# Optimization experiments

Hardware: AMD Instinct MI355X
Metric: run time of the kernel (lower is better)

The kernel has to match this reference:

```python
import jax, jax.numpy as jnp
import numpy as np
from jax import lax

B, T, PRED_LEN = 1024, 100, 30
E, H, IN = 512, 1024, 2


def _gru_cell(h, gx, Whh, bhh):
    # PyTorch GRU cell. gx = x @ Wih.T + bih precomputed, shape (B, 3H).
    gh = h @ Whh.T + bhh
    gx_r, gx_z, gx_n = jnp.split(gx, 3, axis=-1)
    gh_r, gh_z, gh_n = jnp.split(gh, 3, axis=-1)
    r = jax.nn.sigmoid(gx_r + gh_r)
    z = jax.nn.sigmoid(gx_z + gh_z)
    n = jnp.tanh(gx_n + r * gh_n)
    return (1.0 - z) * n + z * h


def _run_gru(x, h0, Wih, Whh, bih, bhh):
    # x: (B, T, F) -> outputs (B, T, H), final hidden (B, H)
    gx = jnp.einsum('btf,gf->btg', x, Wih) + bih  # batch all input projections
    def step(h, gxt):
        h_new = _gru_cell(h, gxt, Whh, bhh)
        return h_new, h_new
    h_last, ys = lax.scan(step, h0, jnp.swapaxes(gx, 0, 1))
    return jnp.swapaxes(ys, 0, 1), h_last


def setup_inputs() -> dict:
    key = jax.random.key(0)
    ks = iter(jax.random.split(key, 32))
    s = 1.0 / np.sqrt(H)
    u = lambda k, shp: jax.random.uniform(k, shp, jnp.float32, -s, s)
    inp = {'obs': jax.random.normal(next(ks), (B, T, IN), jnp.float32)}
    inp['We'] = u(next(ks), (E, IN)); inp['be'] = u(next(ks), (E,))
    inp['Wed'] = u(next(ks), (E, 2)); inp['bed'] = u(next(ks), (E,))
    for name, fin in [('enc1', E), ('enc2', H), ('dec1', E), ('dec2', H)]:
        inp[name + '_Wih'] = u(next(ks), (3 * H, fin))
        inp[name + '_Whh'] = u(next(ks), (3 * H, H))
        inp[name + '_bih'] = u(next(ks), (3 * H,))
        inp[name + '_bhh'] = u(next(ks), (3 * H,))
    inp['Wout'] = u(next(ks), (2, H)); inp['bout'] = u(next(ks), (2,))
    return inp


def reference(obs, We, be, Wed, bed,
              enc1_Wih, enc1_Whh, enc1_bih, enc1_bhh,
              enc2_Wih, enc2_Whh, enc2_bih, enc2_bhh,
              dec1_Wih, dec1_Whh, dec1_bih, dec1_bhh,
              dec2_Wih, dec2_Whh, dec2_bih, dec2_bhh,
              Wout, bout):
    b = obs.shape[0]
    h0 = jnp.zeros((b, H), obs.dtype)
    # --- encoder ---
    emb = jnp.tanh(jnp.einsum('bti,ei->bte', obs, We) + be)
    enc1, h = _run_gru(emb, h0, enc1_Wih, enc1_Whh, enc1_bih, enc1_bhh)
    # quirk preserved: hidden from gru1 is fed as h0 of gru2
    enc2, h = _run_gru(enc1, h, enc2_Wih, enc2_Whh, enc2_bih, enc2_bhh)
    out_loc0 = enc2[:, -2, :] @ Wout.T + bout  # second-to-last step (B, 2)
    def dec_step(carry, _):
        hc, last = carry
        d_emb = jnp.tanh(last @ Wed.T + bed)
        h1 = _gru_cell(hc, d_emb @ dec1_Wih.T + dec1_bih, dec1_Whh, dec1_bhh)
        h2 = _gru_cell(h1, h1 @ dec2_Wih.T + dec2_bih, dec2_Whh, dec2_bhh)
        out = h2 @ Wout.T + bout
        return (h2, out), out
    _, preds = lax.scan(dec_step, (h, out_loc0), None, length=PRED_LEN)
    return jnp.swapaxes(preds, 0, 1)  # (B, pred_len, 2)
```

## Files before the change

### kernel.cpp

```cpp
#include <hip/hip_runtime.h>
#include <stdint.h>

#define NB 1024
#define NT 100
#define NPRED 30
#define NE 512
#define NH 1024
#define NG (3*NH)

typedef unsigned short u16;
typedef unsigned int u32;
typedef u16 u16x4 __attribute__((ext_vector_type(4)));
typedef float f32x4 __attribute__((ext_vector_type(4)));
typedef __bf16 bf16x8 __attribute__((ext_vector_type(8)));

__device__ __forceinline__ u16 f2b(float f){
  u32 u = __float_as_uint(f);
  u = (u + 0x7FFFu + ((u >> 16) & 1u)) >> 16;
  return (u16)u;
}
__device__ __forceinline__ float sig_(float x){ return 1.0f/(1.0f+__expf(-x)); }
__device__ __forceinline__ float tanh_(float x){
  float e = __expf(2.0f*fabsf(x));
  return copysignf(1.0f - 2.0f/(e+1.0f), x);
}

__global__ void cvt_kernel(const float* src, u16* dst, int n4){
  int i = blockIdx.x*256 + threadIdx.x;
  if (i < n4){
    f32x4 v = ((const f32x4*)src)[i];
    u16x4 o;
    o[0]=f2b(v[0]); o[1]=f2b(v[1]); o[2]=f2b(v[2]); o[3]=f2b(v[3]);
    ((u16x4*)dst)[i] = o;
  }
}

__global__ void emb_kernel(const float* __restrict__ obs, const float* __restrict__ We,
                           const float* __restrict__ be, u16* __restrict__ out, int t){
  int idx = blockIdx.x*256 + threadIdx.x;
  int b = idx >> 9, e = idx & 511;
  float x0 = obs[(b*NT + t)*2], x1 = obs[(b*NT + t)*2 + 1];
  out[idx] = f2b(tanh_(We[e*2]*x0 + We[e*2+1]*x1 + be[e]));
}

__global__ void demb_kernel(const float* __restrict__ last, const float* __restrict__ Wed,
                            const float* __restrict__ bed, u16* __restrict__ out){
  int idx = blockIdx.x*256 + threadIdx.x;
  int b = idx >> 9, e = idx & 511;
  out[idx] = f2b(tanh_(Wed[e*2]*last[b*2] + Wed[e*2+1]*last[b*2+1] + bed[e]));
}

__device__ __forceinline__ void gload16(const u16* g, const u16* lds){
  __builtin_amdgcn_global_load_lds(
      (const __attribute__((address_space(1))) void*)g,
      (__attribute__((address_space(3))) void*)lds, 16, 0, 0);
}

__device__ __forceinline__ void gemm_tile_body(
    const u16* __restrict__ A, int lda,
    const u16* __restrict__ W, int K,
    const float* __restrict__ bias, float* __restrict__ C,
    int bRow, int bCol)
{
  __shared__ __align__(16) u16 As[2][128][64];
  __shared__ __align__(16) u16 Bs[2][128][64];

  const int tid = threadIdx.x;
  const int w = tid >> 6, l = tid & 63;
  const int wm = w >> 1, wn = w & 1;
  const int fr = l & 15, lhi = l >> 4;
  const int srow = l >> 3;
  const int gcol = (((l & 7) ^ srow) * 8);

  f32x4 acc[4][4];
  #pragma unroll
  for (int m=0;m<4;m++)
    #pragma unroll
    for (int n=0;n<4;n++) acc[m][n] = (f32x4)0.0f;

  const u16* Ab = A + (size_t)bRow*lda + gcol;
  const u16* Wb = W + (size_t)bCol*K + gcol;
  const int NK = K >> 6;

  #pragma unroll
  for (int s4=0;s4<4;s4++){
    int slab = w*4 + s4;
    int row = slab*8 + srow;
    gload16(Ab + (size_t)row*lda, &As[0][slab*8][0]);
    gload16(Wb + (size_t)row*K,   &Bs[0][slab*8][0]);
  }
  __syncthreads();

  for (int t = 0; t < NK; ++t){
    const int cur = t & 1;
    if (t + 1 < NK){
      const int k0 = (t+1)*64;
      #pragma unroll
      for (int s4=0;s4<4;s4++){
        int slab = w*4 + s4;
        int row = slab*8 + srow;
        gload16(Ab + (size_t)row*lda + k0, &As[cur^1][slab*8][0]);
        gload16(Wb + (size_t)row*K   + k0, &Bs[cur^1][slab*8][0]);
      }
    }
    const u16* Ac = &As[cur][0][0];
    const u16* Bc = &Bs[cur][0][0];
    #pragma unroll
    for (int kk=0; kk<2; ++kk){
      const int ch = (((kk*4 + lhi) ^ (l & 7)) * 8);
      bf16x8 af[4], bfr[4];
      #pragma unroll
      for (int m=0;m<4;m++)
        af[m] = *(const bf16x8*)(Ac + (size_t)(wm*64 + m*16 + fr)*64 + ch);
      #pragma unroll
      for (int n=0;n<4;n++)
        bfr[n] = *(const bf16x8*)(Bc + (size_t)(wn*64 + n*16 + fr)*64 + ch);
      #pragma unroll
      for (int m=0;m<4;m++)
        #pragma unroll
        for (int n=0;n<4;n++)
          acc[m][n] = __builtin_amdgcn_mfma_f32_16x16x32_bf16(af[m], bfr[n], acc[m][n], 0, 0, 0);
    }
    __syncthreads();
  }

  const int crow = lhi * 4, ccol = l & 15;
  #pragma unroll
  for (int n=0;n<4;n++){
    int col = bCol + wn*64 + n*16 + ccol;
    float bv = bias[col];
    #pragma unroll
    for (int m=0;m<4;m++){
      int row = bRow + wm*64 + m*16 + crow;
      float* Cp = C + (size_t)row*NG + col;
      #pragma unroll
      for (int r=0;r<4;r++) Cp[(size_t)r*NG] = acc[m][n][r] + bv;
    }
  }
}

__global__ __launch_bounds__(256)
void gemm_dual_kernel(
  const u16* A0, int lda0, int K0, const u16* W0, const float* bias0, float* C0,
  const u16* A1, int lda1, int K1, const u16* W1, const float* bias1, float* C1)
{
  if (blockIdx.z == 0)
    gemm_tile_body(A0, lda0, W0, K0, bias0, C0, blockIdx.y*128, blockIdx.x*128);
  else
    gemm_tile_body(A1, lda1, W1, K1, bias1, C1, blockIdx.y*128, blockIdx.x*128);
}

__global__ void gru_cell_kernel(const float* __restrict__ gx, const float* __restrict__ gh,
                                const float* __restrict__ hin, float* __restrict__ hout,
                                u16* __restrict__ houtb, u16* __restrict__ seq)
{
  int idx = blockIdx.x*256 + threadIdx.x;
  int b = idx >> 8, jq = idx & 255;
  int base = b*768;
  const f32x4* gx4 = (const f32x4*)gx;
  const f32x4* gh4 = (const f32x4*)gh;
  f32x4 xr = gx4[base + jq], xz = gx4[base + 256 + jq], xn = gx4[base + 512 + jq];
  f32x4 hr = gh4[base + jq], hz = gh4[base + 256 + jq], hn = gh4[base + 512 + jq];
  f32x4 hv = ((const f32x4*)hin)[idx];
  f32x4 o; u16x4 ob;
  #pragma unroll
  for (int c=0;c<4;c++){
    float r = sig_(xr[c] + hr[c]);
    float z = sig_(xz[c] + hz[c]);
    float n = tanh_(xn[c] + r*hn[c]);
    float h = (1.0f - z)*n + z*hv[c];
    o[c] = h; ob[c] = f2b(h);
  }
  ((f32x4*)hout)[idx] = o;
  ((u16x4*)houtb)[idx] = ob;
  if (seq) ((u16x4*)seq)[idx] = ob;
}

__global__ void outproj_kernel(const float* __restrict__ h, const float* __restrict__ Wout,
                               const float* __restrict__ bout, float* __restrict__ last,
                               float* __restrict__ dout, int t)
{
  int b = blockIdx.x, tid = threadIdx.x;
  float s0 = 0.f, s1 = 0.f;
  const float* hb_ = h + (size_t)b*NH;
  for (int j = tid; j < NH; j += 256){
    float hv = hb_[j];
    s0 += hv * Wout[j];
    s1 += hv * Wout[NH + j];
  }
  #pragma unroll
  for (int off = 32; off > 0; off >>= 1){
    s0 += __shfl_down(s0, off);
    s1 += __shfl_down(s1, off);
  }
  __shared__ float red[8];
  int w = tid >> 6;
  if ((tid & 63) == 0){ red[w*2] = s0; red[w*2+1] = s1; }
  __syncthreads();
  if (tid == 0){
    float o0 = red[0]+red[2]+red[4]+red[6] + bout[0];
    float o1 = red[1]+red[3]+red[5]+red[7] + bout[1];
    last[b*2]   = o0;
    last[b*2+1] = o1;
    if (dout){ dout[(size_t)b*(NPRED*2) + t*2]     = o0;
               dout[(size_t)b*(NPRED*2) + t*2 + 1] = o1; }
  }
}

extern "C" void kernel_launch(void* const* d_in, const int* in_sizes, int n_in,
                              void* d_out, int out_size, void* d_ws, size_t ws_size,
                              hipStream_t stream)
{
  (void)in_sizes; (void)n_in; (void)out_size;
  const float* obs  = (const float*)d_in[0];
  const float* We   = (const float*)d_in[1];
  const float* be   = (const float*)d_in[2];
  const float* Wed  = (const float*)d_in[3];
  const float* bed  = (const float*)d_in[4];
  const float* e1Wih = (const float*)d_in[5];
  const float* e1Whh = (const float*)d_in[6];
  const float* e1bih = (const float*)d_in[7];
  const float* e1bhh = (const float*)d_in[8];
  const float* e2Wih = (const float*)d_in[9];
  const float* e2Whh = (const float*)d_in[10];
  const float* e2bih = (const float*)d_in[11];
  const float* e2bhh = (const float*)d_in[12];
  const float* d1Wih = (const float*)d_in[13];
  const float* d1Whh = (const float*)d_in[14];
  const float* d1bih = (const float*)d_in[15];
  const float* d1bhh = (const float*)d_in[16];
  const float* d2Wih = (const float*)d_in[17];
  const float* d2Whh = (const float*)d_in[18];
  const float* d2bih = (const float*)d_in[19];
  const float* d2bhh = (const float*)d_in[20];
  const float* Wout = (const float*)d_in[21];
  const float* bout = (const float*)d_in[22];
  float* out = (float*)d_out;

  char* ws = (char*)d_ws;
  size_t off = 0;
  auto alloc = [&](size_t bytes)->char* {
    char* p = ws + off;
    off += (bytes + 255) & ~(size_t)255;
    return p;
  };
  u16* wE1i = (u16*)alloc((size_t)NG*NE*2);
  u16* wE1h = (u16*)alloc((size_t)NG*NH*2);
  u16* wE2i = (u16*)alloc((size_t)NG*NH*2);
  u16* wE2h = (u16*)alloc((size_t)NG*NH*2);
  u16* wD1i = (u16*)alloc((size_t)NG*NE*2);
  u16* wD1h = (u16*)alloc((size_t)NG*NH*2);
  u16* wD2i = (u16*)alloc((size_t)NG*NH*2);
  u16* wD2h = (u16*)alloc((size_t)NG*NH*2);
  u16* embb  = (u16*)alloc((size_t)NB*NE*2);
  float* h1f = (float*)alloc((size_t)NB*NH*4);
  u16*   h1b = (u16*)alloc((size_t)NB*NH*2);
  float* h2f = (float*)alloc((size_t)NB*NH*4);
  u16*   h2b = (u16*)alloc((size_t)NB*NH*2);
  float* gx  = (float*)alloc((size_t)NB*NG*4);
  float* gh  = (float*)alloc((size_t)NB*NG*4);
  float* last = (float*)alloc((size_t)NB*2*4);

  const size_t slot = (size_t)NB*NH*2;
  size_t avail = (ws_size > off + (1u<<20)) ? (ws_size - off - (1u<<20)) : 0;
  int cs = (int)(avail / slot);
  if (cs > NT) cs = NT;
  u16* cache = (u16*)alloc((size_t)cs * slot);
  const int cache_start = NT - cs;

  hipMemsetAsync(h1f, 0, (size_t)NB*NH*4, stream);
  hipMemsetAsync(h1b, 0, (size_t)NB*NH*2, stream);

  auto cvt = [&](const float* src, u16* dst, size_t n){
    int n4 = (int)(n >> 2);
    cvt_kernel<<<dim3((n4 + 255)/256), dim3(256), 0, stream>>>(src, dst, n4);
  };
  cvt(e1Wih, wE1i, (size_t)NG*NE);
  cvt(e1Whh, wE1h, (size_t)NG*NH);
  cvt(e2Wih, wE2i, (size_t)NG*NH);
  cvt(e2Whh, wE2h, (size_t)NG*NH);
  cvt(d1Wih, wD1i, (size_t)NG*NE);
  cvt(d1Whh, wD1h, (size_t)NG*NH);
  cvt(d2Wih, wD2i, (size_t)NG*NH);
  cvt(d2Whh, wD2h, (size_t)NG*NH);

  const dim3 blk(256);
  const dim3 dual_grid(NG/128, NB/128, 2);
  const dim3 emb_grid((NB*NE)/256);
  const dim3 cell_grid((NB*NH/4)/256);

  for (int t = 0; t < NT; ++t){
    emb_kernel<<<emb_grid, blk, 0, stream>>>(obs, We, be, embb, t);
    gemm_dual_kernel<<<dual_grid, blk, 0, stream>>>(
        embb, NE, NE, wE1i, e1bih, gx,
        h1b,  NH, NH, wE1h, e1bhh, gh);
    u16* slot_p = (t >= cache_start) ? cache + (size_t)(t - cache_start)*NB*NH : (u16*)nullptr;
    gru_cell_kernel<<<cell_grid, blk, 0, stream>>>(gx, gh, h1f, h1f, h1b, slot_p);
  }

  hipMemcpyAsync(h2f, h1f, (size_t)NB*NH*4, hipMemcpyDeviceToDevice, stream);
  hipMemcpyAsync(h2b, h1b, (size_t)NB*NH*2, hipMemcpyDeviceToDevice, stream);

  if (cache_start > 0){
    hipMemsetAsync(h1f, 0, (size_t)NB*NH*4, stream);
    hipMemsetAsync(h1b, 0, (size_t)NB*NH*2, stream);
  }
  for (int t = 0; t < cache_start; ++t){
    emb_kernel<<<emb_grid, blk, 0, stream>>>(obs, We, be, embb, t);
    gemm_dual_kernel<<<dual_grid, blk, 0, stream>>>(
        embb, NE, NE, wE1i, e1bih, gx,
        h1b,  NH, NH, wE1h, e1bhh, gh);
    gru_cell_kernel<<<cell_grid, blk, 0, stream>>>(gx, gh, h1f, h1f, h1b, (u16*)nullptr);
    gemm_dual_kernel<<<dual_grid, blk, 0, stream>>>(
        h1b, NH, NH, wE2i, e2bih, gx,
        h2b, NH, NH, wE2h, e2bhh, gh);
    gru_cell_kernel<<<cell_grid, blk, 0, stream>>>(gx, gh, h2f, h2f, h2b, (u16*)nullptr);
    if (t == NT - 2)
      outproj_kernel<<<dim3(NB), blk, 0, stream>>>(h2f, Wout, bout, last, (float*)nullptr, 0);
  }
  for (int t = cache_start; t < NT; ++t){
    const u16* enc1_t = cache + (size_t)(t - cache_start)*NB*NH;
    gemm_dual_kernel<<<dual_grid, blk, 0, stream>>>(
        enc1_t, NH, NH, wE2i, e2bih, gx,
        h2b,    NH, NH, wE2h, e2bhh, gh);
    gru_cell_kernel<<<cell_grid, blk, 0, stream>>>(gx, gh, h2f, h2f, h2b, (u16*)nullptr);
    if (t == NT - 2)
      outproj_kernel<<<dim3(NB), blk, 0, stream>>>(h2f, Wout, bout, last, (float*)nullptr, 0);
  }

  for (int t = 0; t < NPRED; ++t){
    demb_kernel<<<emb_grid, blk, 0, stream>>>(last, Wed, bed, embb);
    gemm_dual_kernel<<<dual_grid, blk, 0, stream>>>(
        embb, NE, NE, wD1i, d1bih, gx,
        h2b,  NH, NH, wD1h, d1bhh, gh);
    gru_cell_kernel<<<cell_grid, blk, 0, stream>>>(gx, gh, h2f, h1f, h1b, (u16*)nullptr);
    gemm_dual_kernel<<<dual_grid, blk, 0, stream>>>(
        h1b, NH, NH, wD2i, d2bih, gx,
        h1b, NH, NH, wD2h, d2bhh, gh);
    gru_cell_kernel<<<cell_grid, blk, 0, stream>>>(gx, gh, h1f, h2f, h2b, (u16*)nullptr);
    outproj_kernel<<<dim3(NB), blk, 0, stream>>>(h2f, Wout, bout, last, out, t);
  }
}
```

Before: 8.357 ms.

## Use 4-stage K=32 LDS pipeline with vmcnt waits in GEMM tile

Replaces the double-buffered K=64 tile loop with a four-buffer K=32 pipeline that keeps three global-to-LDS loads in flight. Each step uses an explicit s_waitcnt vmcnt plus one barrier instead of two __syncthreads. A new XOR swizzle is applied for the 32-wide rows. The aim is to hide global load latency better in the input-projection GEMMs, at the cost of more barriers per K and fragile hand-counted vmcnt values.

```diff
diff --git a/kernel.cpp b/kernel.cpp
--- a/kernel.cpp
+++ b/kernel.cpp
@@ -62,15 +62,22 @@
     const float* __restrict__ bias, float* __restrict__ C,
     int bRow, int bCol)
 {
-  __shared__ __align__(16) u16 As[2][128][64];
-  __shared__ __align__(16) u16 Bs[2][128][64];
+  __shared__ __align__(16) u16 As[4][128][32];
+  __shared__ __align__(16) u16 Bs[4][128][32];
 
   const int tid = threadIdx.x;
   const int w = tid >> 6, l = tid & 63;
   const int wm = w >> 1, wn = w & 1;
   const int fr = l & 15, lhi = l >> 4;
-  const int srow = l >> 3;
-  const int gcol = (((l & 7) ^ srow) * 8);
+
+  const int srow = l >> 2;
+  const int sch  = (((l & 3) ^ ((l >> 2) & 3) ^ (l >> 4)) << 3);
+  const int s0 = w*2, s1 = w*2 + 1;
+
+  const u16* A0p = A + (size_t)(bRow + s0*16 + srow)*lda + sch;
+  const u16* A1p = A + (size_t)(bRow + s1*16 + srow)*lda + sch;
+  const u16* W0p = W + (size_t)(bCol + s0*16 + srow)*K + sch;
+  const u16* W1p = W + (size_t)(bCol + s1*16 + srow)*K + sch;
 
   f32x4 acc[4][4];
   #pragma unroll
@@ -78,51 +85,55 @@
     #pragma unroll
     for (int n=0;n<4;n++) acc[m][n] = (f32x4)0.0f;
 
-  const u16* Ab = A + (size_t)bRow*lda + gcol;
-  const u16* Wb = W + (size_t)bCol*K + gcol;
-  const int NK = K >> 6;
-
-  #pragma unroll
-  for (int s4=0;s4<4;s4++){
-    int slab = w*4 + s4;
-    int row = slab*8 + srow;
-    gload16(Ab + (size_t)row*lda, &As[0][slab*8][0]);
-    gload16(Wb + (size_t)row*K,   &Bs[0][slab*8][0]);
-  }
-  __syncthreads();
-
-  for (int t = 0; t < NK; ++t){
-    const int cur = t & 1;
-    if (t + 1 < NK){
-      const int k0 = (t+1)*64;
-      #pragma unroll
-      for (int s4=0;s4<4;s4++){
-        int slab = w*4 + s4;
-        int row = slab*8 + srow;
-        gload16(Ab + (size_t)row*lda + k0, &As[cur^1][slab*8][0]);
-        gload16(Wb + (size_t)row*K   + k0, &Bs[cur^1][slab*8][0]);
-      }
-    }
-    const u16* Ac = &As[cur][0][0];
-    const u16* Bc = &Bs[cur][0][0];
-    #pragma unroll
-    for (int kk=0; kk<2; ++kk){
-      const int ch = (((kk*4 + lhi) ^ (l & 7)) * 8);
-      bf16x8 af[4], bfr[4];
-      #pragma unroll
-      for (int m=0;m<4;m++)
-        af[m] = *(const bf16x8*)(Ac + (size_t)(wm*64 + m*16 + fr)*64 + ch);
-      #pragma unroll
-      for (int n=0;n<4;n++)
-        bfr[n] = *(const bf16x8*)(Bc + (size_t)(wn*64 + n*16 + fr)*64 + ch);
-      #pragma unroll
-      for (int m=0;m<4;m++)
-        #pragma unroll
-        for (int n=0;n<4;n++)
-          acc[m][n] = __builtin_amdgcn_mfma_f32_16x16x32_bf16(af[m], bfr[n], acc[m][n], 0, 0, 0);
-    }
-    __syncthreads();
-  }
+  const int rch = ((lhi ^ (fr & 3) ^ (fr >> 2)) << 3);
+
+  #define STAGE(buf, t) do { int _k = (t) << 5; \
+    gload16(A0p + _k, &As[(buf)][s0*16][0]); \
+    gload16(A1p + _k, &As[(buf)][s1*16][0]); \
+    gload16(W0p + _k, &Bs[(buf)][s0*16][0]); \
+    gload16(W1p + _k, &Bs[(buf)][s1*16][0]); } while(0)
+
+  #define COMPUTE(buf) do { \
+    const u16* Ac = &As[(buf)][0][0]; \
+    const u16* Bc = &Bs[(buf)][0][0]; \
+    bf16x8 af[4], bfr[4]; \
+    _Pragma("unroll") \
+    for (int m=0;m<4;m++) af[m]  = *(const bf16x8*)(Ac + (size_t)(wm*64 + m*16 + fr)*32 + rch); \
+    _Pragma("unroll") \
+    for (int n=0;n<4;n++) bfr[n] = *(const bf16x8*)(Bc + (size_t)(wn*64 + n*16 + fr)*32 + rch); \
+    _Pragma("unroll") \
+    for (int m=0;m<4;m++) \
+      _Pragma("unroll") \
+      for (int n=0;n<4;n++) \
+        acc[m][n] = __builtin_amdgcn_mfma_f32_16x16x32_bf16(af[m], bfr[n], acc[m][n], 0, 0, 0); \
+    } while(0)
+
+  const int NK = K >> 5;
+
+  STAGE(0, 0); STAGE(1, 1); STAGE(2, 2);
+
+  for (int t = 0; t + 4 <= NK; ++t){
+    asm volatile("s_waitcnt vmcnt(8)" ::: "memory");
+    __builtin_amdgcn_s_barrier();
+    asm volatile("" ::: "memory");
+    STAGE((t + 3) & 3, t + 3);
+    COMPUTE(t & 3);
+  }
+  asm volatile("s_waitcnt vmcnt(8)" ::: "memory");
+  __builtin_amdgcn_s_barrier();
+  asm volatile("" ::: "memory");
+  COMPUTE((NK - 3) & 3);
+  asm volatile("s_waitcnt vmcnt(4)" ::: "memory");
+  __builtin_amdgcn_s_barrier();
+  asm volatile("" ::: "memory");
+  COMPUTE((NK - 2) & 3);
+  asm volatile("s_waitcnt vmcnt(0)" ::: "memory");
+  __builtin_amdgcn_s_barrier();
+  asm volatile("" ::: "memory");
+  COMPUTE((NK - 1) & 3);
+
+  #undef STAGE
+  #undef COMPUTE
 
   const int crow = lhi * 4, ccol = l & 15;
   #pragma unroll
```

Result: slower. 10.02 ms (+19.9%).

## Fuse GRU gate GEMMs and cell update into one kernel with gate-interleaved weights

Applied to the files above, without the earlier changes.

Weights are repacked so that each 384-column block holds the r, z and n gate rows for the same 128 hidden units. This lets one kernel run both the input and hidden GEMMs into register accumulators and apply the GRU cell in its epilogue. The fp32 gx/gh intermediates and the separate cell kernel go away, and the embedding and decoder-embedding computations are folded into the step and output-projection kernels. Hidden-state buffers are double-buffered to avoid read/write races across blocks. The grid drops to only 128 blocks, each holding 32 accumulators, which may leave much of the GPU idle.

```diff
diff --git a/kernel.cpp b/kernel.cpp
--- a/kernel.cpp
+++ b/kernel.cpp
@@ -25,14 +25,27 @@
   return copysignf(1.0f - 2.0f/(e+1.0f), x);
 }
 
-__global__ void cvt_kernel(const float* src, u16* dst, int n4){
-  int i = blockIdx.x*256 + threadIdx.x;
-  if (i < n4){
-    f32x4 v = ((const f32x4*)src)[i];
-    u16x4 o;
-    o[0]=f2b(v[0]); o[1]=f2b(v[1]); o[2]=f2b(v[2]); o[3]=f2b(v[3]);
-    ((u16x4*)dst)[i] = o;
-  }
+__global__ void pack_w_kernel(const float* __restrict__ src, u16* __restrict__ dst, int K){
+  int idx = blockIdx.x*256 + threadIdx.x;
+  int kq = K >> 2;
+  int rowp = idx / kq, kc = idx % kq;
+  int q = rowp / 48, rem = rowp % 48;
+  int g = rem >> 4, s = rem & 15;
+  int j = q*16 + s;
+  f32x4 v = ((const f32x4*)src)[(size_t)(g*NH + j)*kq + kc];
+  u16x4 o;
+  o[0]=f2b(v[0]); o[1]=f2b(v[1]); o[2]=f2b(v[2]); o[3]=f2b(v[3]);
+  ((u16x4*)dst)[idx] = o;
+}
+
+__global__ void pack_bias_kernel(const float* __restrict__ bih, const float* __restrict__ bhh,
+                                 float* __restrict__ PB1, float* __restrict__ PB2){
+  int idx = blockIdx.x*256 + threadIdx.x;
+  int q = idx / 48, rem = idx % 48;
+  int g = rem >> 4, s = rem & 15;
+  int j = q*16 + s;
+  PB1[idx] = (g < 2) ? (bih[g*NH + j] + bhh[g*NH + j]) : bhh[2*NH + j];
+  if (idx < NH) PB2[idx] = bih[2*NH + idx];
 }
 
 __global__ void emb_kernel(const float* __restrict__ obs, const float* __restrict__ We,
@@ -43,150 +56,147 @@
   out[idx] = f2b(tanh_(We[e*2]*x0 + We[e*2+1]*x1 + be[e]));
 }
 
-__global__ void demb_kernel(const float* __restrict__ last, const float* __restrict__ Wed,
-                            const float* __restrict__ bed, u16* __restrict__ out){
-  int idx = blockIdx.x*256 + threadIdx.x;
-  int b = idx >> 9, e = idx & 511;
-  out[idx] = f2b(tanh_(Wed[e*2]*last[b*2] + Wed[e*2+1]*last[b*2+1] + bed[e]));
-}
-
 __device__ __forceinline__ void gload16(const u16* g, const u16* lds){
   __builtin_amdgcn_global_load_lds(
       (const __attribute__((address_space(1))) void*)g,
       (__attribute__((address_space(3))) void*)lds, 16, 0, 0);
 }
 
-__device__ __forceinline__ void gemm_tile_body(
-    const u16* __restrict__ A, int lda,
-    const u16* __restrict__ W, int K,
-    const float* __restrict__ bias, float* __restrict__ C,
-    int bRow, int bCol)
+template<bool TOX>
+__device__ __forceinline__ void gemm_phase(
+    const u16* __restrict__ A, int lda, int K,
+    const u16* __restrict__ W,
+    int rb, int w, int l,
+    f32x4* acc, f32x4* accx,
+    u16 (*As)[64][64], u16 (*Ws)[384][64])
 {
-  __shared__ __align__(16) u16 As[2][128][64];
-  __shared__ __align__(16) u16 Bs[2][128][64];
-
-  const int tid = threadIdx.x;
-  const int w = tid >> 6, l = tid & 63;
-  const int wm = w >> 1, wn = w & 1;
   const int fr = l & 15, lhi = l >> 4;
   const int srow = l >> 3;
   const int gcol = (((l & 7) ^ srow) * 8);
-
-  f32x4 acc[4][4];
-  #pragma unroll
-  for (int m=0;m<4;m++)
-    #pragma unroll
-    for (int n=0;n<4;n++) acc[m][n] = (f32x4)0.0f;
-
-  const u16* Ab = A + (size_t)bRow*lda + gcol;
-  const u16* Wb = W + (size_t)bCol*K + gcol;
+  const u16* Ab = A + (size_t)(rb*64)*lda + gcol;
+  const u16* Wb = W + gcol;
   const int NK = K >> 6;
 
-  #pragma unroll
-  for (int s4=0;s4<4;s4++){
-    int slab = w*4 + s4;
-    int row = slab*8 + srow;
-    gload16(Ab + (size_t)row*lda, &As[0][slab*8][0]);
-    gload16(Wb + (size_t)row*K,   &Bs[0][slab*8][0]);
-  }
+  #define STAGE_P(buf, kt) do { int _k0 = (kt)*64; \
+    _Pragma("unroll") \
+    for (int c=0;c<2;c++){ int sl = w*2 + c; \
+      gload16(Ab + (size_t)(sl*8+srow)*lda + _k0, &As[(buf)][sl*8][0]); } \
+    _Pragma("unroll") \
+    for (int c=0;c<12;c++){ int sl = w*12 + c; \
+      gload16(Wb + (size_t)(sl*8+srow)*K + _k0, &Ws[(buf)][sl*8][0]); } } while(0)
+
+  STAGE_P(0, 0);
   __syncthreads();
 
   for (int t = 0; t < NK; ++t){
     const int cur = t & 1;
-    if (t + 1 < NK){
-      const int k0 = (t+1)*64;
-      #pragma unroll
-      for (int s4=0;s4<4;s4++){
-        int slab = w*4 + s4;
-        int row = slab*8 + srow;
-        gload16(Ab + (size_t)row*lda + k0, &As[cur^1][slab*8][0]);
-        gload16(Wb + (size_t)row*K   + k0, &Bs[cur^1][slab*8][0]);
-      }
-    }
-    const u16* Ac = &As[cur][0][0];
-    const u16* Bc = &Bs[cur][0][0];
+    if (t + 1 < NK) STAGE_P(cur^1, t+1);
     #pragma unroll
     for (int kk=0; kk<2; ++kk){
       const int ch = (((kk*4 + lhi) ^ (l & 7)) * 8);
-      bf16x8 af[4], bfr[4];
+      bf16x8 af[4], wf[6];
       #pragma unroll
       for (int m=0;m<4;m++)
-        af[m] = *(const bf16x8*)(Ac + (size_t)(wm*64 + m*16 + fr)*64 + ch);
+        af[m] = *(const bf16x8*)(&As[cur][m*16 + fr][0] + ch);
       #pragma unroll
-      for (int n=0;n<4;n++)
-        bfr[n] = *(const bf16x8*)(Bc + (size_t)(wn*64 + n*16 + fr)*64 + ch);
+      for (int nf=0;nf<6;nf++)
+        wf[nf] = *(const bf16x8*)(&Ws[cur][w*96 + nf*16 + fr][0] + ch);
       #pragma unroll
-      for (int m=0;m<4;m++)
+      for (int nf=0;nf<6;nf++)
         #pragma unroll
-        for (int n=0;n<4;n++)
-          acc[m][n] = __builtin_amdgcn_mfma_f32_16x16x32_bf16(af[m], bfr[n], acc[m][n], 0, 0, 0);
+        for (int m=0;m<4;m++){
+          if (TOX && (nf % 3) == 2)
+            accx[(nf/3)*4 + m] = __builtin_amdgcn_mfma_f32_16x16x32_bf16(af[m], wf[nf], accx[(nf/3)*4 + m], 0, 0, 0);
+          else
+            acc[nf*4 + m] = __builtin_amdgcn_mfma_f32_16x16x32_bf16(af[m], wf[nf], acc[nf*4 + m], 0, 0, 0);
+        }
     }
     __syncthreads();
   }
-
-  const int crow = lhi * 4, ccol = l & 15;
-  #pragma unroll
-  for (int n=0;n<4;n++){
-    int col = bCol + wn*64 + n*16 + ccol;
-    float bv = bias[col];
+  #undef STAGE_P
+}
+
+__global__ __launch_bounds__(256)
+void fused_step(
+    const u16* __restrict__ Ax, int ldax, int Kx, const u16* __restrict__ Wx,
+    const u16* __restrict__ Ah, const u16* __restrict__ Wh,
+    const float* __restrict__ PB1, const float* __restrict__ PB2,
+    const float* __restrict__ hin, float* __restrict__ houtf,
+    u16* __restrict__ houtb, u16* __restrict__ seq,
+    const float* __restrict__ obs, const float* __restrict__ We,
+    const float* __restrict__ be, u16* __restrict__ embb, int et)
+{
+  __shared__ __align__(16) u16 As[2][64][64];
+  __shared__ __align__(16) u16 Ws[2][384][64];
+
+  const int rb = blockIdx.x >> 3, cb = blockIdx.x & 7;
+  const int tid = threadIdx.x, w = tid >> 6, l = tid & 63;
+  const int s = l & 15, lhi = l >> 4;
+
+  f32x4 acc[24], accx[8];
+  #pragma unroll
+  for (int i=0;i<24;i++) acc[i] = (f32x4)0.0f;
+  #pragma unroll
+  for (int i=0;i<8;i++) accx[i] = (f32x4)0.0f;
+
+  gemm_phase<true >(Ax, ldax, Kx, Wx + (size_t)(cb*384)*Kx, rb, w, l, acc, accx, As, Ws);
+  gemm_phase<false>(Ah, NH,   NH, Wh + (size_t)(cb*384)*NH, rb, w, l, acc, accx, As, Ws);
+
+  #pragma unroll
+  for (int gi=0; gi<2; ++gi){
+    int j = cb*128 + (2*w + gi)*16 + s;
+    int pbase = cb*384 + w*96 + gi*48 + s;
+    float pbr = PB1[pbase], pbz = PB1[pbase + 16], pbn = PB1[pbase + 32];
+    float pb2 = PB2[j];
     #pragma unroll
     for (int m=0;m<4;m++){
-      int row = bRow + wm*64 + m*16 + crow;
-      float* Cp = C + (size_t)row*NG + col;
       #pragma unroll
-      for (int r=0;r<4;r++) Cp[(size_t)r*NG] = acc[m][n][r] + bv;
+      for (int r=0;r<4;r++){
+        int row = rb*64 + m*16 + lhi*4 + r;
+        size_t hoff = (size_t)row*NH + j;
+        float rpre = acc[(gi*3+0)*4 + m][r] + pbr;
+        float zpre = acc[(gi*3+1)*4 + m][r] + pbz;
+        float nh   = acc[(gi*3+2)*4 + m][r] + pbn;
+        float nx   = accx[gi*4 + m][r] + pb2;
+        float r_ = sig_(rpre), z_ = sig_(zpre);
+        float nn = tanh_(nx + r_*nh);
+        float h = (1.0f - z_)*nn + z_*hin[hoff];
+        houtf[hoff] = h;
+        u16 hb = f2b(h);
+        houtb[hoff] = hb;
+        if (seq) seq[hoff] = hb;
+      }
     }
   }
-}
-
-__global__ __launch_bounds__(256)
-void gemm_dual_kernel(
-  const u16* A0, int lda0, int K0, const u16* W0, const float* bias0, float* C0,
-  const u16* A1, int lda1, int K1, const u16* W1, const float* bias1, float* C1)
-{
-  if (blockIdx.z == 0)
-    gemm_tile_body(A0, lda0, W0, K0, bias0, C0, blockIdx.y*128, blockIdx.x*128);
-  else
-    gemm_tile_body(A1, lda1, W1, K1, bias1, C1, blockIdx.y*128, blockIdx.x*128);
-}
-
-__global__ void gru_cell_kernel(const float* __restrict__ gx, const float* __restrict__ gh,
-                                const float* __restrict__ hin, float* __restrict__ hout,
-                                u16* __restrict__ houtb, u16* __restrict__ seq)
-{
-  int idx = blockIdx.x*256 + threadIdx.x;
-  int b = idx >> 8, jq = idx & 255;
-  int base = b*768;
-  const f32x4* gx4 = (const f32x4*)gx;
-  const f32x4* gh4 = (const f32x4*)gh;
-  f32x4 xr = gx4[base + jq], xz = gx4[base + 256 + jq], xn = gx4[base + 512 + jq];
-  f32x4 hr = gh4[base + jq], hz = gh4[base + 256 + jq], hn = gh4[base + 512 + jq];
-  f32x4 hv = ((const f32x4*)hin)[idx];
-  f32x4 o; u16x4 ob;
-  #pragma unroll
-  for (int c=0;c<4;c++){
-    float r = sig_(xr[c] + hr[c]);
-    float z = sig_(xz[c] + hz[c]);
-    float n = tanh_(xn[c] + r*hn[c]);
-    float h = (1.0f - z)*n + z*hv[c];
-    o[c] = h; ob[c] = f2b(h);
-  }
-  ((f32x4*)hout)[idx] = o;
-  ((u16x4*)houtb)[idx] = ob;
-  if (seq) ((u16x4*)seq)[idx] = ob;
-}
-
-__global__ void outproj_kernel(const float* __restrict__ h, const float* __restrict__ Wout,
-                               const float* __restrict__ bout, float* __restrict__ last,
-                               float* __restrict__ dout, int t)
+
+  if (embb){
+    int row = rb*64 + (tid >> 2);
+    float x0 = obs[((size_t)row*NT + et)*2];
+    float x1 = obs[((size_t)row*NT + et)*2 + 1];
+    #pragma unroll
+    for (int c=0;c<8;c++){
+      int e = cb*64 + ((tid & 3)*8 + c)*2;
+      u16 v0 = f2b(tanh_(We[e*2]  *x0 + We[e*2+1]*x1 + be[e]));
+      u16 v1 = f2b(tanh_(We[e*2+2]*x0 + We[e*2+3]*x1 + be[e+1]));
+      ((u32*)embb)[(size_t)row*256 + cb*32 + (tid & 3)*8 + c] = (u32)v0 | ((u32)v1 << 16);
+    }
+  }
+}
+
+__global__ void outproj_demb_kernel(const float* __restrict__ h,
+                                    const float* __restrict__ Wout, const float* __restrict__ bout,
+                                    float* __restrict__ dout, int ot,
+                                    const float* __restrict__ Wed, const float* __restrict__ bed,
+                                    u16* __restrict__ dembb)
 {
   int b = blockIdx.x, tid = threadIdx.x;
+  f32x4 hv = ((const f32x4*)h)[b*256 + tid];
+  int j0 = tid*4;
   float s0 = 0.f, s1 = 0.f;
-  const float* hb_ = h + (size_t)b*NH;
-  for (int j = tid; j < NH; j += 256){
-    float hv = hb_[j];
-    s0 += hv * Wout[j];
-    s1 += hv * Wout[NH + j];
+  #pragma unroll
+  for (int c=0;c<4;c++){
+    s0 += hv[c]*Wout[j0+c];
+    s1 += hv[c]*Wout[NH + j0 + c];
   }
   #pragma unroll
   for (int off = 32; off > 0; off >>= 1){
@@ -194,17 +204,23 @@
     s1 += __shfl_down(s1, off);
   }
   __shared__ float red[8];
+  __shared__ float lastsh[2];
   int w = tid >> 6;
   if ((tid & 63) == 0){ red[w*2] = s0; red[w*2+1] = s1; }
   __syncthreads();
   if (tid == 0){
     float o0 = red[0]+red[2]+red[4]+red[6] + bout[0];
     float o1 = red[1]+red[3]+red[5]+red[7] + bout[1];
-    last[b*2]   = o0;
-    last[b*2+1] = o1;
-    if (dout){ dout[(size_t)b*(NPRED*2) + t*2]     = o0;
-               dout[(size_t)b*(NPRED*2) + t*2 + 1] = o1; }
-  }
+    lastsh[0] = o0; lastsh[1] = o1;
+    if (dout){ dout[(size_t)b*(NPRED*2) + ot*2]     = o0;
+               dout[(size_t)b*(NPRED*2) + ot*2 + 1] = o1; }
+  }
+  __syncthreads();
+  float x0 = lastsh[0], x1 = lastsh[1];
+  int e0 = tid*2;
+  u16 v0 = f2b(tanh_(Wed[e0*2]  *x0 + Wed[e0*2+1]*x1 + bed[e0]));
+  u16 v1 = f2b(tanh_(Wed[e0*2+2]*x0 + Wed[e0*2+3]*x1 + bed[e0+1]));
+  ((u32*)dembb)[b*256 + tid] = (u32)v0 | ((u32)v1 << 16);
 }
 
 extern "C" void kernel_launch(void* const* d_in, const int* in_sizes, int n_in,
@@ -244,22 +260,24 @@
     off += (bytes + 255) & ~(size_t)255;
     return p;
   };
-  u16* wE1i = (u16*)alloc((size_t)NG*NE*2);
-  u16* wE1h = (u16*)alloc((size_t)NG*NH*2);
-  u16* wE2i = (u16*)alloc((size_t)NG*NH*2);
-  u16* wE2h = (u16*)alloc((size_t)NG*NH*2);
-  u16* wD1i = (u16*)alloc((size_t)NG*NE*2);
-  u16* wD1h = (u16*)alloc((size_t)NG*NH*2);
-  u16* wD2i = (u16*)alloc((size_t)NG*NH*2);
-  u16* wD2h = (u16*)alloc((size_t)NG*NH*2);
-  u16* embb  = (u16*)alloc((size_t)NB*NE*2);
+  u16* pE1i = (u16*)alloc((size_t)NG*NE*2);
+  u16* pE1h = (u16*)alloc((size_t)NG*NH*2);
+  u16* pE2i = (u16*)alloc((size_t)NG*NH*2);
+  u16* pE2h = (u16*)alloc((size_t)NG*NH*2);
+  u16* pD1i = (u16*)alloc((size_t)NG*NE*2);
+  u16* pD1h = (u16*)alloc((size_t)NG*NH*2);
+  u16* pD2i = (u16*)alloc((size_t)NG*NH*2);
+  u16* pD2h = (u16*)alloc((size_t)NG*NH*2);
+  float* PB1e1 = (float*)alloc(NG*4); float* PB2e1 = (float*)alloc(NH*4);
+  float* PB1e2 = (float*)alloc(NG*4); float* PB2e2 = (float*)alloc(NH*4);
+  float* PB1d1 = (float*)alloc(NG*4); float* PB2d1 = (float*)alloc(NH*4);
+  float* PB1d2 = (float*)alloc(NG*4); float* PB2d2 = (float*)alloc(NH*4);
+  u16* embbP[2] = { (u16*)alloc((size_t)NB*NE*2), (u16*)alloc((size_t)NB*NE*2) };
+  u16* dembb = (u16*)alloc((size_t)NB*NE*2);
   float* h1f = (float*)alloc((size_t)NB*NH*4);
-  u16*   h1b = (u16*)alloc((size_t)NB*NH*2);
+  u16*   h1bP[2] = { (u16*)alloc((size_t)NB*NH*2), (u16*)alloc((size_t)NB*NH*2) };
   float* h2f = (float*)alloc((size_t)NB*NH*4);
-  u16*   h2b = (u16*)alloc((size_t)NB*NH*2);
-  float* gx  = (float*)alloc((size_t)NB*NG*4);
-  float* gh  = (float*)alloc((size_t)NB*NG*4);
-  float* last = (float*)alloc((size_t)NB*2*4);
+  u16*   h2bP[2] = { (u16*)alloc((size_t)NB*NH*2), (u16*)alloc((size_t)NB*NH*2) };
 
   const size_t slot = (size_t)NB*NH*2;
   size_t avail = (ws_size > off + (1u<<20)) ? (ws_size - off - (1u<<20)) : 0;
@@ -269,75 +287,86 @@
   const int cache_start = NT - cs;
 
   hipMemsetAsync(h1f, 0, (size_t)NB*NH*4, stream);
-  hipMemsetAsync(h1b, 0, (size_t)NB*NH*2, stream);
-
-  auto cvt = [&](const float* src, u16* dst, size_t n){
-    int n4 = (int)(n >> 2);
-    cvt_kernel<<<dim3((n4 + 255)/256), dim3(256), 0, stream>>>(src, dst, n4);
+  hipMemsetAsync(h1bP[0], 0, (size_t)NB*NH*2, stream);
+
+  const dim3 blk(256);
+  auto packw = [&](const float* src, u16* dst, int K){
+    pack_w_kernel<<<dim3((NG*K/4)/256), blk, 0, stream>>>(src, dst, K);
   };
-  cvt(e1Wih, wE1i, (size_t)NG*NE);
-  cvt(e1Whh, wE1h, (size_t)NG*NH);
-  cvt(e2Wih, wE2i, (size_t)NG*NH);
-  cvt(e2Whh, wE2h, (size_t)NG*NH);
-  cvt(d1Wih, wD1i, (size_t)NG*NE);
-  cvt(d1Whh, wD1h, (size_t)NG*NH);
-  cvt(d2Wih, wD2i, (size_t)NG*NH);
-  cvt(d2Whh, wD2h, (size_t)NG*NH);
-
-  const dim3 blk(256);
-  const dim3 dual_grid(NG/128, NB/128, 2);
+  packw(e1Wih, pE1i, NE); packw(e1Whh, pE1h, NH);
+  packw(e2Wih, pE2i, NH); packw(e2Whh, pE2h, NH);
+  packw(d1Wih, pD1i, NE); packw(d1Whh, pD1h, NH);
+  packw(d2Wih, pD2i, NH); packw(d2Whh, pD2h, NH);
+  pack_bias_kernel<<<dim3(NG/256), blk, 0, stream>>>(e1bih, e1bhh, PB1e1, PB2e1);
+  pack_bias_kernel<<<dim3(NG/256), blk, 0, stream>>>(e2bih, e2bhh, PB1e2, PB2e2);
+  pack_bias_kernel<<<dim3(NG/256), blk, 0, stream>>>(d1bih, d1bhh, PB1d1, PB2d1);
+  pack_bias_kernel<<<dim3(NG/256), blk, 0, stream>>>(d2bih, d2bhh, PB1d2, PB2d2);
+
+  const dim3 fgrid(128);
   const dim3 emb_grid((NB*NE)/256);
-  const dim3 cell_grid((NB*NH/4)/256);
-
+
+  int p1 = 0, p2 = 0, pe = 0;
+
+  emb_kernel<<<emb_grid, blk, 0, stream>>>(obs, We, be, embbP[0], 0);
   for (int t = 0; t < NT; ++t){
-    emb_kernel<<<emb_grid, blk, 0, stream>>>(obs, We, be, embb, t);
-    gemm_dual_kernel<<<dual_grid, blk, 0, stream>>>(
-        embb, NE, NE, wE1i, e1bih, gx,
-        h1b,  NH, NH, wE1h, e1bhh, gh);
     u16* slot_p = (t >= cache_start) ? cache + (size_t)(t - cache_start)*NB*NH : (u16*)nullptr;
-    gru_cell_kernel<<<cell_grid, blk, 0, stream>>>(gx, gh, h1f, h1f, h1b, slot_p);
+    u16* embn = (t + 1 < NT) ? embbP[pe^1] : (u16*)nullptr;
+    fused_step<<<fgrid, blk, 0, stream>>>(
+        embbP[pe], NE, NE, pE1i, h1bP[p1], pE1h, PB1e1, PB2e1,
+        h1f, h1f, h1bP[p1^1], slot_p,
+        obs, We, be, embn, t+1);
+    p1 ^= 1; pe ^= 1;
   }
 
   hipMemcpyAsync(h2f, h1f, (size_t)NB*NH*4, hipMemcpyDeviceToDevice, stream);
-  hipMemcpyAsync(h2b, h1b, (size_t)NB*NH*2, hipMemcpyDeviceToDevice, stream);
+  hipMemcpyAsync(h2bP[0], h1bP[p1], (size_t)NB*NH*2, hipMemcpyDeviceToDevice, stream);
+  p2 = 0;
 
   if (cache_start > 0){
     hipMemsetAsync(h1f, 0, (size_t)NB*NH*4, stream);
-    hipMemsetAsync(h1b, 0, (size_t)NB*NH*2, stream);
+    hipMemsetAsync(h1bP[0], 0, (size_t)NB*NH*2, stream);
+    p1 = 0; pe = 0;
+    emb_kernel<<<emb_grid, blk, 0, stream>>>(obs, We, be, embbP[0], 0);
   }
   for (int t = 0; t < cache_start; ++t){
-    emb_kernel<<<emb_grid, blk, 0, stream>>>(obs, We, be, embb, t);
-    gemm_dual_kernel<<<dual_grid, blk, 0, stream>>>(
-        embb, NE, NE, wE1i, e1bih, gx,
-        h1b,  NH, NH, wE1h, e1bhh, gh);
-    gru_cell_kernel<<<cell_grid, blk, 0, stream>>>(gx, gh, h1f, h1f, h1b, (u16*)nullptr);
-    gemm_dual_kernel<<<dual_grid, blk, 0, stream>>>(
-        h1b, NH, NH, wE2i, e2bih, gx,
-        h2b, NH, NH, wE2h, e2bhh, gh);
-    gru_cell_kernel<<<cell_grid, blk, 0, stream>>>(gx, gh, h2f, h2f, h2b, (u16*)nullptr);
+    u16* embn = (t + 1 < cache_start) ? embbP[pe^1] : (u16*)nullptr;
+    fused_step<<<fgrid, blk, 0, stream>>>(
+        embbP[pe], NE, NE, pE1i, h1bP[p1], pE1h, PB1e1, PB2e1,
+        h1f, h1f, h1bP[p1^1], (u16*)nullptr,
+        obs, We, be, embn, t+1);
+    p1 ^= 1; pe ^= 1;
+    fused_step<<<fgrid, blk, 0, stream>>>(
+        h1bP[p1], NH, NH, pE2i, h2bP[p2], pE2h, PB1e2, PB2e2,
+        h2f, h2f, h2bP[p2^1], (u16*)nullptr,
+        nullptr, nullptr, nullptr, nullptr, 0);
+    p2 ^= 1;
     if (t == NT - 2)
-      outproj_kernel<<<dim3(NB), blk, 0, stream>>>(h2f, Wout, bout, last, (float*)nullptr, 0);
+      outproj_demb_kernel<<<dim3(NB), blk, 0, stream>>>(
+          h2f, Wout, bout, (float*)nullptr, 0, Wed, bed, dembb);
   }
   for (int t = cache_start; t < NT; ++t){
     const u16* enc1_t = cache + (size_t)(t - cache_start)*NB*NH;
-    gemm_dual_kernel<<<dual_grid, blk, 0, stream>>>(
-        enc1_t, NH, NH, wE2i, e2bih, gx,
-        h2b,    NH, NH, wE2h, e2bhh, gh);
-    gru_cell_kernel<<<cell_grid, blk, 0, stream>>>(gx, gh, h2f, h2f, h2b, (u16*)nullptr);
+    fused_step<<<fgrid, blk, 0, stream>>>(
+        enc1_t, NH, NH, pE2i, h2bP[p2], pE2h, PB1e2, PB2e2,
+        h2f, h2f, h2bP[p2^1], (u16*)nullptr,
+        nullptr, nullptr, nullptr, nullptr, 0);
+    p2 ^= 1;
     if (t == NT - 2)
-      outproj_kernel<<<dim3(NB), blk, 0, stream>>>(h2f, Wout, bout, last, (float*)nullptr, 0);
+      outproj_demb_kernel<<<dim3(NB), blk, 0, stream>>>(
+          h2f, Wout, bout, (float*)nullptr, 0, Wed, bed, dembb);
   }
 
   for (int t = 0; t < NPRED; ++t){
-    demb_kernel<<<emb_grid, blk, 0, stream>>>(last, Wed, bed, embb);
-    gemm_dual_kernel<<<dual_grid, blk, 0, stream>>>(
-        embb, NE, NE, wD1i, d1bih, gx,
-        h2b,  NH, NH, wD1h, d1bhh, gh);
-    gru_cell_kernel<<<cell_grid, blk, 0, stream>>>(gx, gh, h2f, h1f, h1b, (u16*)nullptr);
-    gemm_dual_kernel<<<dual_grid, blk, 0, stream>>>(
-        h1b, NH, NH, wD2i, d2bih, gx,
-        h1b, NH, NH, wD2h, d2bhh, gh);
-    gru_cell_kernel<<<cell_grid, blk, 0, stream>>>(gx, gh, h1f, h2f, h2b, (u16*)nullptr);
-    outproj_kernel<<<dim3(NB), blk, 0, stream>>>(h2f, Wout, bout, last, out, t);
-  }
-}
+    fused_step<<<fgrid, blk, 0, stream>>>(
+        dembb, NE, NE, pD1i, h2bP[p2], pD1h, PB1d1, PB2d1,
+        h2f, h1f, h1bP[0], (u16*)nullptr,
+        nullptr, nullptr, nullptr, nullptr, 0);
+    fused_step<<<fgrid, blk, 0, stream>>>(
+        h1bP[0], NH, NH, pD2i, h1bP[0], pD2h, PB1d2, PB2d2,
+        h1f, h2f, h2bP[p2^1], (u16*)nullptr,
+        nullptr, nullptr, nullptr, nullptr, 0);
+    p2 ^= 1;
+    outproj_demb_kernel<<<dim3(NB), blk, 0, stream>>>(
+        h2f, Wout, bout, out, t, Wed, bed, dembb);
+  }
+}
```

Measured after the change: 12.62 ms. +51.0%, slower.
